# Kernel optimization log

Hardware: AMD Instinct MI355X
Metric: run time of the kernel (lower is better)

The kernel has to match this reference:

```python
import jax, jax.numpy as jnp
import numpy as np

STAGES = [80, 40, 20]
INPUT = 640
NUM_CLASSES = 80
B = 32
PRE_NMS = 1000      # top-k candidates fed to NMS (fixed-shape surrogate for full sort)
MAX_DET = 100       # max_num_detections
IOU_TH = 0.5
CLASS_OFF = 4096.0  # batched_nms trick: offset boxes per class so classes never overlap


def setup_inputs() -> dict:
    key = jax.random.key(0)
    ks = jax.random.split(key, 6)
    inp = {}
    for i, s in enumerate(STAGES):
        inp[f"cls{i}"] = jax.random.normal(ks[2 * i], (B, NUM_CLASSES, s, s), dtype=jnp.float32)
        # positive ltrb distances, up to ~64 px
        inp[f"box{i}"] = jax.random.uniform(ks[2 * i + 1], (B, 4, s, s), dtype=jnp.float32) * 64.0
    return inp


def _decode_level(cls, box, stage):
    # cls: [B,C,H,W], box: [B,4,H,W]
    step = INPUT // stage
    cls = jax.nn.sigmoid(jnp.transpose(cls, (0, 2, 3, 1)))   # [B,H,W,C]
    conf = jnp.max(cls, axis=-1)                             # [B,H,W]
    cidx = jnp.argmax(cls, axis=-1)                          # [B,H,W]
    box = jnp.transpose(box, (0, 2, 3, 1))                   # [B,H,W,4]
    grid = jnp.arange(stage, dtype=box.dtype) * step
    gx, gy = jnp.meshgrid(grid, grid, indexing='xy')
    block = jnp.stack([gx, gy], axis=-1)                     # [H,W,2]
    xy1 = block - box[..., :2]
    xy2 = block + box[..., 2:4]
    boxes = jnp.concatenate([xy1, xy2], axis=-1).reshape(box.shape[0], -1, 4)
    return boxes, conf.reshape(conf.shape[0], -1), cidx.reshape(cidx.shape[0], -1)


def _iou_matrix(b):
    # b: [N,4] -> [N,N] pairwise IoU
    area = jnp.maximum(b[:, 2] - b[:, 0], 0.) * jnp.maximum(b[:, 3] - b[:, 1], 0.)
    lt = jnp.maximum(b[:, None, :2], b[None, :, :2])
    rb = jnp.minimum(b[:, None, 2:], b[None, :, 2:])
    wh = jnp.maximum(rb - lt, 0.)
    inter = wh[..., 0] * wh[..., 1]
    return inter / (area[:, None] + area[None, :] - inter + 1e-7)


def _nms_image(boxes, scores, classes):
    # class-aware (batched) NMS via per-class coordinate offset
    off = classes.astype(boxes.dtype) * CLASS_OFF
    ob = boxes + off[:, None]
    s_top, idx = jax.lax.top_k(scores, PRE_NMS)
    b_top = ob[idx]                                          # [PRE,4], score-sorted desc
    iou = _iou_matrix(b_top)
    ar = jnp.arange(PRE_NMS)

    def body(i, supp):
        row = (iou[i] > IOU_TH) & (ar > i)
        return jnp.where(supp[i], supp, supp | row)

    supp = jax.lax.fori_loop(0, PRE_NMS, body, jnp.zeros((PRE_NMS,), bool))
    kept_scores = jnp.where(supp, -jnp.inf, s_top)
    sel_s, sel = jax.lax.top_k(kept_scores, MAX_DET)
    final = idx[sel]                                         # indices into original 8400
    valid = jnp.isfinite(sel_s)
    out_b = jnp.where(valid[:, None], boxes[final], 0.)
    out_s = jnp.where(valid, scores[final], 0.)
    out_c = jnp.where(valid, classes[final], -1)
    return out_b, out_s, out_c


def reference(cls0, box0, cls1, box1, cls2, box2):
    parts = [_decode_level(c, b, s) for c, b, s in
             zip([cls0, cls1, cls2], [box0, box1, box2], STAGES)]
    boxes = jnp.concatenate([p[0] for p in parts], axis=1)    # [B,8400,4]
    scores = jnp.concatenate([p[1] for p in parts], axis=1)   # [B,8400]
    classes = jnp.concatenate([p[2] for p in parts], axis=1)  # [B,8400]
    ob, os_, oc = jax.vmap(_nms_image)(boxes, scores, classes)
    boxes_with_scores = jnp.concatenate([ob, os_[..., None]], axis=-1)  # [B,MAX_DET,5]
    return boxes_with_scores, oc
```

## Files before the change

kernel.cpp:

```cpp
#include <hip/hip_runtime.h>

typedef unsigned int u32;
typedef unsigned long long u64;

#define NB 32
#define NCLS 80
#define NANCHOR 8400
#define PRE 1000
#define MAXDET 100
#define NT 1024

__global__ void decode_kernel(const float* __restrict__ cls0, const float* __restrict__ box0,
                              const float* __restrict__ cls1, const float* __restrict__ box1,
                              const float* __restrict__ cls2, const float* __restrict__ box2,
                              float* __restrict__ ws_scores, float4* __restrict__ ws_boxes,
                              int* __restrict__ ws_cls) {
    int g = blockIdx.x * blockDim.x + threadIdx.x;
    if (g >= NB * NANCHOR) return;
    int b = g / NANCHOR;
    int r = g - b * NANCHOR;

    const float* cp; const float* bp;
    int HW, hw, h, w, step;
    if (r < 6400) {
        cp = cls0 + (size_t)b * NCLS * 6400; bp = box0 + (size_t)b * 4 * 6400;
        HW = 6400; hw = r;        h = hw / 80; w = hw - h * 80; step = 8;
    } else if (r < 8000) {
        cp = cls1 + (size_t)b * NCLS * 1600; bp = box1 + (size_t)b * 4 * 1600;
        HW = 1600; hw = r - 6400; h = hw / 40; w = hw - h * 40; step = 16;
    } else {
        cp = cls2 + (size_t)b * NCLS * 400;  bp = box2 + (size_t)b * 4 * 400;
        HW = 400;  hw = r - 8000; h = hw / 20; w = hw - h * 20; step = 32;
    }

    float m = cp[hw];
    int ci = 0;
    for (int c = 1; c < NCLS; ++c) {
        float v = cp[(size_t)c * HW + hw];
        if (v > m) { m = v; ci = c; }
    }
    float score = 1.0f / (1.0f + expf(-m));

    float l = bp[hw], t = bp[HW + hw], rr = bp[2 * HW + hw], bo = bp[3 * HW + hw];
    float gx = (float)(w * step), gy = (float)(h * step);

    ws_scores[g] = score;
    ws_boxes[g] = make_float4(gx - l, gy - t, gx + rr, gy + bo);
    ws_cls[g] = ci;
}

__device__ __forceinline__ u64 shfl_xor_u64(u64 v, int m) {
    u32 lo = (u32)v, hi = (u32)(v >> 32);
    lo = (u32)__shfl_xor((int)lo, m, 64);
    hi = (u32)__shfl_xor((int)hi, m, 64);
    return ((u64)hi << 32) | (u64)lo;
}

__device__ __forceinline__ u64 readlane_u64(u64 v, int l) {
    u32 lo = (u32)v, hi = (u32)(v >> 32);
    lo = (u32)__builtin_amdgcn_readlane((int)lo, l);
    hi = (u32)__builtin_amdgcn_readlane((int)hi, l);
    return ((u64)hi << 32) | (u64)lo;
}

__device__ __forceinline__ void suffix_scan_1024(int* sh, int* swsum, int* swadd) {
    const int tid = threadIdx.x, lane = tid & 63, wv = tid >> 6;
    int s = sh[tid];
#pragma unroll
    for (int off = 1; off < 64; off <<= 1) {
        int u = __shfl_down(s, off, 64);
        if (lane + off < 64) s += u;
    }
    if (lane == 0) swsum[wv] = s;
    __syncthreads();
    if (tid < 64) {
        int t = (lane < 16) ? swsum[lane] : 0;
#pragma unroll
        for (int off = 1; off < 16; off <<= 1) {
            int u = __shfl_down(t, off, 64);
            if (lane + off < 64) t += u;
        }
        int ab = __shfl_down(t, 1, 64);
        if (lane < 16) swadd[lane] = (lane == 15) ? 0 : ab;
    }
    __syncthreads();
    sh[tid] = s + swadd[wv];
    __syncthreads();
}

__global__ __launch_bounds__(NT) void select_sort_kernel(
        const float* __restrict__ ws_scores, const float4* __restrict__ ws_boxes,
        const int* __restrict__ ws_cls, u64* __restrict__ ws_keys,
        float* __restrict__ ws_sx1, float* __restrict__ ws_sy1,
        float* __restrict__ ws_sx2, float* __restrict__ ws_sy2,
        float* __restrict__ ws_sar) {
    const int b = blockIdx.x;
    const int tid = threadIdx.x;

    __shared__ u32 s_sb[NANCHOR];
    __shared__ int s_hist[1024];
    __shared__ u64 s_key[2048];
    __shared__ int s_wsum[16], s_wadd[16];
    __shared__ int s_C, s_base, s_cnt;
    __shared__ u32 s_thresh;

    const float* sc = ws_scores + (size_t)b * NANCHOR;

    s_hist[tid] = 0;
    s_key[tid] = 0ULL;
    s_key[tid + 1024] = 0ULL;
    if (tid == 0) s_cnt = 0;
    __syncthreads();

    for (int a = tid; a < NANCHOR; a += NT) {
        u32 sb = __float_as_uint(sc[a]);
        s_sb[a] = sb;
        atomicAdd(&s_hist[sb >> 20], 1);
    }
    __syncthreads();
    suffix_scan_1024(s_hist, s_wsum, s_wadd);
    {
        int sfx = s_hist[tid];
        int nxt = (tid < 1023) ? s_hist[tid + 1] : 0;
        if (sfx >= PRE && (tid == 1023 || nxt < PRE)) { s_C = tid; s_base = nxt; }
    }
    __syncthreads();
    const int C = s_C, base = s_base;
    s_hist[tid] = 0;
    __syncthreads();

    for (int a = tid; a < NANCHOR; a += NT) {
        u32 sb = s_sb[a];
        if ((int)(sb >> 20) == C) atomicAdd(&s_hist[(sb >> 10) & 1023], 1);
    }
    __syncthreads();
    suffix_scan_1024(s_hist, s_wsum, s_wadd);
    {
        int sfx = base + s_hist[tid];
        int nxt = base + ((tid < 1023) ? s_hist[tid + 1] : 0);
        if (sfx >= PRE && (tid == 1023 || nxt < PRE))
            s_thresh = ((u32)C << 20) | ((u32)tid << 10);
    }
    __syncthreads();
    const u32 thresh = s_thresh;

    for (int a = tid; a < NANCHOR; a += NT) {
        u32 sb = s_sb[a];
        if (sb >= thresh) {
            int pos = atomicAdd(&s_cnt, 1);
            if (pos < 2048)
                s_key[pos] = ((u64)sb << 14) | (u64)(NANCHOR - 1 - a);
        }
    }
    __syncthreads();
    const int cnt = s_cnt;
    const int sortN = (cnt <= 1024) ? 1024 : 2048;

    bool prevBig = false;
    for (int k = 2; k <= sortN; k <<= 1) {
        for (int j = k >> 1; j > 0; j >>= 1) {
            const bool big = (j >= 64);
            if (big || prevBig) __syncthreads();
            else __builtin_amdgcn_wave_barrier();
            for (int i = tid; i < sortN; i += NT) {
                int ixj = i ^ j;
                if (ixj > i) {
                    u64 va = s_key[i], vb = s_key[ixj];
                    bool desc = ((i & k) == 0);
                    if (desc ? (va < vb) : (va > vb)) { s_key[i] = vb; s_key[ixj] = va; }
                }
            }
            prevBig = big;
        }
    }
    __syncthreads();

    {
        u64 key = s_key[tid];
        ws_keys[(b << 10) + tid] = key;
        int idx = (NANCHOR - 1) - (int)(key & 16383ULL);
        float4 bx = ws_boxes[(size_t)b * NANCHOR + idx];
        int c = ws_cls[(size_t)b * NANCHOR + idx];
        float off = (float)c * 4096.0f;
        float x1 = bx.x + off, y1 = bx.y + off, x2 = bx.z + off, y2 = bx.w + off;
        int o = (b << 10) + tid;
        ws_sx1[o] = x1; ws_sy1[o] = y1; ws_sx2[o] = x2; ws_sy2[o] = y2;
        ws_sar[o] = fmaxf(x2 - x1, 0.0f) * fmaxf(y2 - y1, 0.0f);
    }
}

__global__ __launch_bounds__(1024) void iou_bits_kernel(
        const float* __restrict__ ws_sx1, const float* __restrict__ ws_sy1,
        const float* __restrict__ ws_sx2, const float* __restrict__ ws_sy2,
        const float* __restrict__ ws_sar,
        u64* __restrict__ ws_bits, u64* __restrict__ ws_diag) {
    const int blk = blockIdx.x;
    const int b = blk >> 4, tile = blk & 15;
    const int tid = threadIdx.x;

    __shared__ float sx1[1024], sy1[1024], sx2[1024], sy2[1024], sar[1024];
    {
        int o = (b << 10) + tid;
        sx1[tid] = ws_sx1[o]; sy1[tid] = ws_sy1[o];
        sx2[tid] = ws_sx2[o]; sy2[tid] = ws_sy2[o];
        sar[tid] = ws_sar[o];
    }
    __syncthreads();

    const int rl = tid & 63, w = tid >> 6;
    const int r = (tile << 6) + rl;
    u64 bits = 0ULL;
    if (r < 1000 && w >= tile) {
        float xi1 = sx1[r], yi1 = sy1[r], xi2 = sx2[r], yi2 = sy2[r], ai = sar[r];
        const int jbase = w << 6;
#pragma unroll 8
        for (int kb = 0; kb < 64; ++kb) {
            int j = jbase + kb;
            float lx = fmaxf(xi1, sx1[j]);
            float ly = fmaxf(yi1, sy1[j]);
            float rx = fminf(xi2, sx2[j]);
            float ry = fminf(yi2, sy2[j]);
            float wx = fmaxf(rx - lx, 0.0f);
            float wy = fmaxf(ry - ly, 0.0f);
            float inter = wx * wy;
            float iou = inter / (ai + sar[j] - inter + 1e-7f);
            bits |= (iou > 0.5f) ? (1ULL << kb) : 0ULL;
        }
        u64 mlow;
        if (w == tile) {
            int bpos = r & 63;
            mlow = (bpos == 63) ? 0ULL : (~0ULL << (bpos + 1));
        } else mlow = ~0ULL;
        u64 mhigh = (jbase + 64 <= 1000) ? ~0ULL : ((1ULL << (1000 - jbase)) - 1ULL);
        bits &= mlow & mhigh;
    }
    ws_bits[((size_t)b << 14) + ((size_t)r << 4) + w] = bits;
    if (w == tile) ws_diag[(b << 10) + r] = bits;
}

__global__ __launch_bounds__(128) void nms_scan_kernel(
        const u64* __restrict__ ws_bits, const u64* __restrict__ ws_diag,
        const u64* __restrict__ ws_keys, const float4* __restrict__ ws_boxes,
        const int* __restrict__ ws_cls, float* __restrict__ out) {
    const int b = blockIdx.x;
    const int tid = threadIdx.x;

    __shared__ int s_keep[MAXDET];
    __shared__ int s_nk;

    if (tid < 64) {
        const int lane = tid;
        const u64* bits = ws_bits + ((size_t)b << 14);
        const u64* diag = ws_diag + ((size_t)b << 10);
        int nkept = 0;
        for (int wi = 0; wi < 16 && nkept < MAXDET; ++wi) {
            const int wbase = wi << 6;
            u64 acc = 0ULL;
            if (lane < nkept)       acc  = bits[((size_t)s_keep[lane] << 4) + wi];
            if (lane + 64 < nkept)  acc |= bits[((size_t)s_keep[lane + 64] << 4) + wi];
#pragma unroll
            for (int off = 32; off > 0; off >>= 1) acc |= shfl_xor_u64(acc, off);
            u64 cur = acc;
            u64 rw = diag[wbase + lane];
            const int nb = (wbase + 64 <= 1000) ? 64 : (1000 - wbase);
            for (int bit = 0; bit < nb; ++bit) {
                if (!((cur >> bit) & 1ULL)) {
                    if (lane == 0) s_keep[nkept] = wbase + bit;
                    nkept++;
                    if (nkept >= MAXDET) break;
                    cur |= readlane_u64(rw, bit);
                }
            }
        }
        if (lane == 0) s_nk = nkept;
    }
    __syncthreads();

    const int nk = s_nk;
    if (tid < MAXDET) {
        float* o = out + ((size_t)b * MAXDET + tid) * 5;
        float* oc = out + (size_t)NB * MAXDET * 5 + (size_t)b * MAXDET + tid;
        if (tid < nk) {
            int rank = s_keep[tid];
            u64 key = ws_keys[(b << 10) + rank];
            int idx = (NANCHOR - 1) - (int)(key & 16383ULL);
            float score = __uint_as_float((u32)(key >> 14));
            float4 bx = ws_boxes[(size_t)b * NANCHOR + idx];
            int c = ws_cls[(size_t)b * NANCHOR + idx];
            o[0] = bx.x; o[1] = bx.y; o[2] = bx.z; o[3] = bx.w; o[4] = score;
            *oc = (float)c;
        } else {
            o[0] = 0.0f; o[1] = 0.0f; o[2] = 0.0f; o[3] = 0.0f; o[4] = 0.0f;
            *oc = -1.0f;
        }
    }
}

extern "C" void kernel_launch(void* const* d_in, const int* in_sizes, int n_in,
                              void* d_out, int out_size, void* d_ws, size_t ws_size,
                              hipStream_t stream) {
    const float* cls0 = (const float*)d_in[0];
    const float* box0 = (const float*)d_in[1];
    const float* cls1 = (const float*)d_in[2];
    const float* box1 = (const float*)d_in[3];
    const float* cls2 = (const float*)d_in[4];
    const float* box2 = (const float*)d_in[5];

    float* ws = (float*)d_ws;
    float* ws_scores = ws;
    float4* ws_boxes = (float4*)(ws + NB * NANCHOR);
    int* ws_cls = (int*)(ws + (size_t)NB * NANCHOR * 5);
    float* base6 = ws + (size_t)NB * NANCHOR * 6;
    u64* ws_keys = (u64*)base6;
    float* ws_sx1 = base6 + 65536;
    float* ws_sy1 = ws_sx1 + NB * 1024;
    float* ws_sx2 = ws_sy1 + NB * 1024;
    float* ws_sy2 = ws_sx2 + NB * 1024;
    float* ws_sar = ws_sy2 + NB * 1024;
    u64* ws_bits = (u64*)(ws_sar + NB * 1024);
    u64* ws_diag = ws_bits + (size_t)NB * 1024 * 16;

    int total = NB * NANCHOR;
    decode_kernel<<<(total + 255) / 256, 256, 0, stream>>>(
        cls0, box0, cls1, box1, cls2, box2, ws_scores, ws_boxes, ws_cls);

    select_sort_kernel<<<NB, NT, 0, stream>>>(ws_scores, ws_boxes, ws_cls, ws_keys,
                                              ws_sx1, ws_sy1, ws_sx2, ws_sy2, ws_sar);

    iou_bits_kernel<<<NB * 16, 1024, 0, stream>>>(ws_sx1, ws_sy1, ws_sx2, ws_sy2, ws_sar,
                                                  ws_bits, ws_diag);

    nms_scan_kernel<<<NB, 128, 0, stream>>>(ws_bits, ws_diag, ws_keys, ws_boxes, ws_cls,
                                            (float*)d_out);
}
```

Measured before the change: 187.0 us.

## Sort 1024 candidate keys in registers of a single wave with shuffles

```diff
diff --git a/kernel.cpp b/kernel.cpp
--- a/kernel.cpp
+++ b/kernel.cpp
@@ -154,26 +154,76 @@
     }
     __syncthreads();
     const int cnt = s_cnt;
-    const int sortN = (cnt <= 1024) ? 1024 : 2048;
-
-    bool prevBig = false;
-    for (int k = 2; k <= sortN; k <<= 1) {
-        for (int j = k >> 1; j > 0; j >>= 1) {
-            const bool big = (j >= 64);
-            if (big || prevBig) __syncthreads();
-            else __builtin_amdgcn_wave_barrier();
-            for (int i = tid; i < sortN; i += NT) {
-                int ixj = i ^ j;
-                if (ixj > i) {
-                    u64 va = s_key[i], vb = s_key[ixj];
-                    bool desc = ((i & k) == 0);
-                    if (desc ? (va < vb) : (va > vb)) { s_key[i] = vb; s_key[ixj] = va; }
+
+    if (cnt > 1024) {
+        bool prevBig = false;
+        for (int k = 2; k <= 2048; k <<= 1) {
+            for (int j = k >> 1; j > 0; j >>= 1) {
+                const bool big = (j >= 64);
+                if (big || prevBig) __syncthreads();
+                else __builtin_amdgcn_wave_barrier();
+                for (int i = tid; i < 2048; i += NT) {
+                    int ixj = i ^ j;
+                    if (ixj > i) {
+                        u64 va = s_key[i], vb = s_key[ixj];
+                        bool desc = ((i & k) == 0);
+                        if (desc ? (va < vb) : (va > vb)) { s_key[i] = vb; s_key[ixj] = va; }
+                    }
+                }
+                prevBig = big;
+            }
+        }
+        __syncthreads();
+    } else {
+        if (tid < 64) {
+            const int lane = tid;
+            u64 v[16];
+#pragma unroll
+            for (int r = 0; r < 16; ++r) v[r] = s_key[(r << 6) | lane];
+
+#define CE_REG(ra, rb, DESC) { u64 a_ = v[(ra)], b_ = v[(rb)];                        \
+            if ((DESC) ? (a_ < b_) : (a_ > b_)) { v[(ra)] = b_; v[(rb)] = a_; } }
+#define CE_SHFL(rr_, jj_, DESC) { u64 a_ = v[(rr_)]; u64 p_ = shfl_xor_u64(a_, (jj_)); \
+            bool up_ = ((lane & (jj_)) == 0); bool km_ = ((DESC) == up_);              \
+            bool pg_ = (p_ > a_); v[(rr_)] = (km_ == pg_) ? p_ : a_; }
+
+#pragma unroll
+            for (int kl = 1; kl <= 10; ++kl) {
+                const int K = 1 << kl;
+#pragma unroll
+                for (int js = 10; js >= 0; --js) {
+                    if (js > kl - 1) continue;
+                    const int j = 1 << js;
+                    if (j >= 64) {
+                        const int jr = j >> 6;
+#pragma unroll
+                        for (int r = 0; r < 16; ++r) {
+                            if ((r & jr) == 0) {
+                                const bool desc = ((r & (K >> 6)) == 0);
+                                CE_REG(r, r | jr, desc);
+                            }
+                        }
+                    } else {
+#pragma unroll
+                        for (int r = 0; r < 16; ++r) {
+                            if (K >= 64) {
+                                const bool desc = ((r & (K >> 6)) == 0);
+                                CE_SHFL(r, j, desc);
+                            } else {
+                                CE_SHFL(r, j, ((lane & K) == 0));
+                            }
+                        }
+                    }
                 }
             }
-            prevBig = big;
-        }
-    }
-    __syncthreads();
+#undef CE_REG
+#undef CE_SHFL
+
+#pragma unroll
+            for (int r = 0; r < 16; ++r) s_key[(r << 6) | lane] = v[r];
+        }
+        __syncthreads();
+    }
 
     {
         u64 key = s_key[tid];
```

Measured after the change: 190.0 us. No clear change (+1.6%).
